# Kernel tuning notes

Hardware: AMD Instinct MI355X
Metric: run time of the kernel (lower is better)

Reference implementation:

```python
import jax, jax.numpy as jnp
import numpy as np

DIM = 1024
HEAD = 16
HEAD_DIM = DIM // HEAD
SCALE = HEAD_DIM ** -0.5
EPS = 1e-5


def layernorm(x, g, b):
    mu = jnp.mean(x, axis=-1, keepdims=True)
    var = jnp.var(x, axis=-1, keepdims=True)
    return (x - mu) * jax.lax.rsqrt(var + EPS) * g + b


def setup_inputs() -> dict:
    key = jax.random.key(0)
    ks = jax.random.split(key, 12)
    B, L = 2, 2048
    s = 0.02
    inp = {
        "x": jax.random.normal(ks[0], (B, L, DIM), jnp.float32),
        "seq_mask": jnp.zeros((B, L), jnp.bool_),
        "wq": jax.random.normal(ks[1], (DIM, DIM), jnp.float32) * s,
        "wk": jax.random.normal(ks[2], (DIM, DIM), jnp.float32) * s,
        "wv": jax.random.normal(ks[3], (DIM, DIM), jnp.float32) * s,
        "wo": jax.random.normal(ks[4], (DIM, DIM), jnp.float32) * s,
        "g1": jnp.ones((DIM,), jnp.float32),
        "b1": jnp.zeros((DIM,), jnp.float32),
        "g2": jnp.ones((DIM,), jnp.float32),
        "b2": jnp.zeros((DIM,), jnp.float32),
        "w_mlp1": jax.random.normal(ks[5], (4 * DIM, DIM), jnp.float32) * s,
        "b_mlp1": jnp.zeros((4 * DIM,), jnp.float32),
        "w_mlp2": jax.random.normal(ks[6], (DIM, 4 * DIM), jnp.float32) * s,
        "b_mlp2": jnp.zeros((DIM,), jnp.float32),
    }
    return inp


def reference(x, seq_mask, wq, wk, wv, wo, g1, b1, g2, b2, w_mlp1, b_mlp1, w_mlp2, b_mlp2):
    B, L, D = x.shape
    # --- pre-norm attention ---
    nx = layernorm(x, g1, b1)
    # torch Linear: y = x @ W.T
    q = (nx @ wq.T).reshape(B, L, HEAD, HEAD_DIM).transpose(0, 2, 1, 3)  # [B,H,L,d]
    k = (nx @ wk.T).reshape(B, L, HEAD, HEAD_DIM).transpose(0, 2, 1, 3)
    v = (nx @ wv.T).reshape(B, L, HEAD, HEAD_DIM).transpose(0, 2, 1, 3)
    scores = jnp.einsum("bhqd,bhkd->bhqk", q, k) * SCALE  # [B,H,L,L]
    causal = jnp.triu(jnp.ones((L, L), jnp.bool_), k=1)  # True = masked
    mask = causal[None, :, :] | seq_mask[:, None, :]      # [B,L,L]
    scores = jnp.where(mask[:, None, :, :], -10000.0, scores)
    attn = jax.nn.softmax(scores, axis=-1)
    out = jnp.einsum("bhqk,bhkd->bhqd", attn, v)
    out = out.transpose(0, 2, 1, 3).reshape(B, L, D)
    attn_out = out @ wo.T
    x = x + attn_out
    # --- pre-norm MLP ---
    nx = layernorm(x, g2, b2)
    h = jax.nn.gelu(nx @ w_mlp1.T + b_mlp1, approximate=False)
    mlp_out = h @ w_mlp2.T + b_mlp2
    return x + mlp_out
```

## Files before the change

### kernel.cpp

```cpp
#include <hip/hip_runtime.h>
#include <hip/hip_bf16.h>
#include <math.h>


#define DIMN 1024
#define NHEAD 16
#define HDIM 64
#define SEQ 2048
#define NTOK 4096
#define QKV_N 3072
#define PADW 72

typedef float v4f __attribute__((ext_vector_type(4)));
typedef short v8s __attribute__((ext_vector_type(8)));

__device__ __forceinline__ float b2f(unsigned short u) {
    union { unsigned int i; float f; } v; v.i = ((unsigned int)u) << 16; return v.f;
}
__device__ __forceinline__ unsigned short f2b(float f) {
    union { float f; unsigned int i; } v; v.f = f;
    unsigned int u = v.i;
    return (unsigned short)((u + 0x7fffu + ((u >> 16) & 1u)) >> 16);
}
__device__ __forceinline__ ushort4 f4tob4(float4 f) {
    ushort4 u; u.x = f2b(f.x); u.y = f2b(f.y); u.z = f2b(f.z); u.w = f2b(f.w); return u;
}
__device__ __forceinline__ void gl2lds16(const unsigned short* g, unsigned short* l) {
    __builtin_amdgcn_global_load_lds(
        (const __attribute__((address_space(1))) unsigned int*)g,
        (__attribute__((address_space(3))) unsigned int*)l, 16, 0, 0);
}

__global__ __launch_bounds__(256) void cast_w_kernel(
    const float* __restrict__ in, unsigned short* __restrict__ out)
{
    size_t i = ((size_t)blockIdx.x * 256 + threadIdx.x) * 8;
    float4 f0 = *(const float4*)(in + i);
    float4 f1 = *(const float4*)(in + i + 4);
    *(ushort4*)(out + i)     = f4tob4(f0);
    *(ushort4*)(out + i + 4) = f4tob4(f1);
}

__global__ __launch_bounds__(256) void concat_w_kernel(
    const float* __restrict__ wq, const float* __restrict__ wk,
    const float* __restrict__ wv, unsigned short* __restrict__ wqkv)
{
    size_t i = ((size_t)blockIdx.x * 256 + threadIdx.x) * 8;
    int which = (int)(i >> 20);
    size_t m = i & ((size_t)(1 << 20) - 1);
    const float* src = (which == 0) ? wq : (which == 1) ? wk : wv;
    float4 f0 = *(const float4*)(src + m);
    float4 f1 = *(const float4*)(src + m + 4);
    *(ushort4*)(wqkv + i)     = f4tob4(f0);
    *(ushort4*)(wqkv + i + 4) = f4tob4(f1);
}

__global__ __launch_bounds__(256) void ln_kernel(
    const float* __restrict__ xin, const float* __restrict__ g,
    const float* __restrict__ b, unsigned short* __restrict__ y)
{
    const int row = blockIdx.x;
    const int t = threadIdx.x;
    float4 u = *((const float4*)(xin + (size_t)row * DIMN) + t);
    float v[4] = {u.x, u.y, u.z, u.w};
    float s1 = v[0] + v[1] + v[2] + v[3];
    float s2 = v[0]*v[0] + v[1]*v[1] + v[2]*v[2] + v[3]*v[3];
    #pragma unroll
    for (int m = 32; m >= 1; m >>= 1) { s1 += __shfl_xor(s1, m); s2 += __shfl_xor(s2, m); }
    __shared__ float a1[4], a2[4];
    const int wave = t >> 6;
    if ((t & 63) == 0) { a1[wave] = s1; a2[wave] = s2; }
    __syncthreads();
    const float S1 = a1[0] + a1[1] + a1[2] + a1[3];
    const float S2 = a2[0] + a2[1] + a2[2] + a2[3];
    const float mean = S1 * (1.0f / DIMN);
    const float var  = S2 * (1.0f / DIMN) - mean * mean;
    const float rinv = rsqrtf(fmaxf(var, 0.0f) + 1e-5f);
    float4 gv = *((const float4*)g + t);
    float4 bv = *((const float4*)b + t);
    ushort4 o;
    o.x = f2b((v[0] - mean) * rinv * gv.x + bv.x);
    o.y = f2b((v[1] - mean) * rinv * gv.y + bv.y);
    o.z = f2b((v[2] - mean) * rinv * gv.z + bv.z);
    o.w = f2b((v[3] - mean) * rinv * gv.w + bv.w);
    *(ushort4*)(y + (size_t)row * DIMN + t * 4) = o;
}

__global__ __launch_bounds__(256) void vtrans_kernel(
    const unsigned short* __restrict__ qkv, unsigned short* __restrict__ vt)
{
    __shared__ unsigned short T[64 * PADW];
    const int st = blockIdx.x;
    const int bh = blockIdx.y;
    const int bb = bh >> 4, h = bh & 15;
    const int t = threadIdx.x;
    const int sr = t >> 2, sc = (t & 3) * 16;
    {
        const unsigned short* g = qkv + (size_t)(bb * SEQ + st * 64 + sr) * QKV_N
                                  + 2 * DIMN + h * HDIM + sc;
        *(uint4*)&T[sr * PADW + sc]     = *(const uint4*)g;
        *(uint4*)&T[sr * PADW + sc + 8] = *(const uint4*)(g + 8);
    }
    __syncthreads();
    {
        const int dr = t >> 2, ss = (t & 3) * 16;
        union { uint4 u; unsigned short s[8]; } o0, o1;
        #pragma unroll
        for (int j = 0; j < 8; j++) o0.s[j] = T[(ss + j) * PADW + dr];
        #pragma unroll
        for (int j = 0; j < 8; j++) o1.s[j] = T[(ss + 8 + j) * PADW + dr];
        unsigned short* dst = vt + ((size_t)bh * 64 + dr) * SEQ + st * 64 + ss;
        *(uint4*)dst       = o0.u;
        *(uint4*)(dst + 8) = o1.u;
    }
}

template<int BN, bool BIAS, bool GELU_ACT, bool RESF32, int OUT>
__global__ __launch_bounds__(256) void gemm_bt_kernel(
    const unsigned short* __restrict__ A, const unsigned short* __restrict__ W,
    const float* __restrict__ bias, const float* __restrict__ resid,
    void* __restrict__ Cout, int M, int N, int K, int LDW)
{
    constexpr int PSA = 128 * 32;
    constexpr int PSB = BN * 32;
    constexpr int TM  = (BN == 128) ? 4 : 2;
    __shared__ unsigned short As[2 * PSA];
    __shared__ unsigned short Bs[2 * PSB];
    const int t = threadIdx.x;
    const int bm = blockIdx.x, bn = blockIdx.y;
    const int wave = t >> 6, lane = t & 63;
    const int lrow = lane & 15, quad = lane >> 4;
    const int wm = (BN == 128) ? (wave & 1) * 64 : wave * 32;
    const int wn = (BN == 128) ? (wave >> 1) * 64 : 0;

    const unsigned short* Ag = A + (size_t)(bm * 128 + (t >> 2)) * K   + (t & 3) * 8;
    const unsigned short* Wg = W + (size_t)(bn * BN  + (t >> 2)) * LDW + (t & 3) * 8;

    v4f acc[TM][4];
    const v4f vzero = {0.f, 0.f, 0.f, 0.f};
    #pragma unroll
    for (int i = 0; i < TM; i++)
        #pragma unroll
        for (int j = 0; j < 4; j++) acc[i][j] = vzero;

    for (int kt = 0; kt < K; kt += 64) {
        gl2lds16(Ag + kt,                        &As[t * 8]);
        gl2lds16(Ag + (size_t)64 * K + kt,       &As[2048 + t * 8]);
        gl2lds16(Ag + kt + 32,                   &As[PSA + t * 8]);
        gl2lds16(Ag + (size_t)64 * K + kt + 32,  &As[PSA + 2048 + t * 8]);
        if constexpr (BN == 128) {
            gl2lds16(Wg + kt,                         &Bs[t * 8]);
            gl2lds16(Wg + (size_t)64 * LDW + kt,      &Bs[2048 + t * 8]);
            gl2lds16(Wg + kt + 32,                    &Bs[PSB + t * 8]);
            gl2lds16(Wg + (size_t)64 * LDW + kt + 32, &Bs[PSB + 2048 + t * 8]);
        } else {
            gl2lds16(Wg + kt,      &Bs[t * 8]);
            gl2lds16(Wg + kt + 32, &Bs[PSB + t * 8]);
        }
        __syncthreads();
        #pragma unroll
        for (int p = 0; p < 2; p++) {
            v8s a[TM], b[4];
            #pragma unroll
            for (int tm = 0; tm < TM; tm++)
                a[tm] = *(const v8s*)&As[p * PSA + (wm + tm * 16 + lrow) * 32 + quad * 8];
            #pragma unroll
            for (int tn = 0; tn < 4; tn++)
                b[tn] = *(const v8s*)&Bs[p * PSB + (wn + tn * 16 + lrow) * 32 + quad * 8];
            #pragma unroll
            for (int tm = 0; tm < TM; tm++)
                #pragma unroll
                for (int tn = 0; tn < 4; tn++)
                    acc[tm][tn] = __builtin_amdgcn_mfma_f32_16x16x32_bf16(
                        a[tm], b[tn], acc[tm][tn], 0, 0, 0);
        }
        __syncthreads();
    }

    #pragma unroll
    for (int tm = 0; tm < TM; tm++) {
        #pragma unroll
        for (int r = 0; r < 4; r++) {
            const int row = bm * 128 + wm + tm * 16 + quad * 4 + r;
            #pragma unroll
            for (int tn = 0; tn < 4; tn++) {
                const int col = bn * BN + wn + tn * 16 + lrow;
                float v = acc[tm][tn][r];
                if (BIAS) v += bias[col];
                if (GELU_ACT) v = 0.5f * v * (1.0f + erff(v * 0.70710678118654752f));
                if (RESF32) v += resid[(size_t)row * N + col];
                if (OUT == 0) ((unsigned short*)Cout)[(size_t)row * N + col] = f2b(v);
                else          ((float*)Cout)[(size_t)row * N + col] = v;
            }
        }
    }
}

__global__ __launch_bounds__(256, 4) void attn_kernel(
    const unsigned short* __restrict__ qkv, const unsigned short* __restrict__ vt,
    unsigned short* __restrict__ aout)
{
    __shared__ unsigned short Qs [64 * PADW];
    __shared__ unsigned short Ks [64 * PADW];
    __shared__ unsigned short Vts[64 * PADW];
    __shared__ unsigned short Ps [64 * PADW];

    const int bh = blockIdx.x;
    const int qt = 31 - blockIdx.y;
    const int bb = bh >> 4, h = bh & 15;
    const int q0 = qt * 64;
    const int t = threadIdx.x;
    const int wave = t >> 6, lane = t & 63;
    const int lrow = lane & 15, quad = lane >> 4;
    const int wq0 = wave * 16;
    const int rotl = (lrow >> 2) & 3;

    const int sr = t >> 2;
    const int sc = (t & 3) * 16;

    {
        const unsigned short* g = qkv + (size_t)(bb * SEQ + q0 + sr) * QKV_N + h * HDIM + sc;
        *(uint4*)&Qs[sr * PADW + sc]     = *(const uint4*)g;
        *(uint4*)&Qs[sr * PADW + sc + 8] = *(const uint4*)(g + 8);
    }

    const unsigned short* kbase = qkv + (size_t)(bb * SEQ + sr) * QKV_N + DIMN + h * HDIM + sc;
    const unsigned short* vbase = vt + ((size_t)bh * 64 + sr) * SEQ + sc;
    uint4 kf0 = *(const uint4*)kbase;
    uint4 kf1 = *(const uint4*)(kbase + 8);
    uint4 vf0 = *(const uint4*)vbase;
    uint4 vf1 = *(const uint4*)(vbase + 8);

    const v4f vzero = {0.f, 0.f, 0.f, 0.f};
    v4f oacc[4], oaccl;
    #pragma unroll
    for (int d = 0; d < 4; d++) oacc[d] = vzero;
    oaccl = vzero;
    v8s bones;
    #pragma unroll
    for (int j = 0; j < 8; j++) bones[j] = (short)0x3F80;

    for (int kti = 0; kti <= qt; kti++) {
        const int kt = kti * 64;
        __syncthreads();
        *(uint4*)&Ks[sr * PADW + sc]      = kf0;
        *(uint4*)&Ks[sr * PADW + sc + 8]  = kf1;
        *(uint4*)&Vts[sr * PADW + sc]     = vf0;
        *(uint4*)&Vts[sr * PADW + sc + 8] = vf1;
        __syncthreads();
        if (kti < qt) {
            const unsigned short* kn = kbase + (size_t)(kti + 1) * 64 * QKV_N;
            const unsigned short* vn = vbase + (kti + 1) * 64;
            kf0 = *(const uint4*)kn;
            kf1 = *(const uint4*)(kn + 8);
            vf0 = *(const uint4*)vn;
            vf1 = *(const uint4*)(vn + 8);
        }

        v8s kb[2][4];
        #pragma unroll
        for (int ks2 = 0; ks2 < 2; ks2++)
            #pragma unroll
            for (int n = 0; n < 4; n++)
                kb[ks2][n] = *(const v8s*)&Ks[(n * 16 + lrow) * PADW + ks2 * 32 + quad * 8];
        v4f sacc[4];
        #pragma unroll
        for (int n = 0; n < 4; n++) sacc[n] = vzero;
        #pragma unroll
        for (int ks2 = 0; ks2 < 2; ks2++) {
            v8s a = *(const v8s*)&Qs[(wq0 + lrow) * PADW + ks2 * 32 + quad * 8];
            #pragma unroll
            for (int n = 0; n < 4; n++)
                sacc[n] = __builtin_amdgcn_mfma_f32_16x16x32_bf16(
                    a, kb[ks2][n], sacc[n], 0, 0, 0);
        }

        const bool diag = (kti == qt);
        #pragma unroll
        for (int n = 0; n < 4; n++) {
            #pragma unroll
            for (int r = 0; r < 4; r++) {
                float e = __expf(fminf(sacc[n][r] * 0.125f, 24.0f));
                if (diag && (n * 16 + lrow) > (wq0 + quad * 4 + r)) e = 0.0f;
                Ps[(wq0 + quad * 4 + r) * PADW + ((n + quad) & 3) * 16 + lrow] = f2b(e);
            }
        }

        v8s vb[2][4];
        #pragma unroll
        for (int ks2 = 0; ks2 < 2; ks2++)
            #pragma unroll
            for (int d = 0; d < 4; d++)
                vb[ks2][d] = *(const v8s*)&Vts[(d * 16 + lrow) * PADW + ks2 * 32 + quad * 8];
        #pragma unroll
        for (int ks2 = 0; ks2 < 2; ks2++) {
            const int kb16 = ks2 * 2 + (quad >> 1);
            v8s a = *(const v8s*)&Ps[(wq0 + lrow) * PADW
                                     + ((kb16 + rotl) & 3) * 16 + (quad & 1) * 8];
            #pragma unroll
            for (int d = 0; d < 4; d++)
                oacc[d] = __builtin_amdgcn_mfma_f32_16x16x32_bf16(
                    a, vb[ks2][d], oacc[d], 0, 0, 0);
            oaccl = __builtin_amdgcn_mfma_f32_16x16x32_bf16(a, bones, oaccl, 0, 0, 0);
        }
    }

    __syncthreads();
    #pragma unroll
    for (int r = 0; r < 4; r++) {
        const float rinv = 1.0f / oaccl[r];
        #pragma unroll
        for (int d = 0; d < 4; d++)
            Qs[(wq0 + quad * 4 + r) * PADW + d * 16 + lrow] = f2b(oacc[d][r] * rinv);
    }
    __syncthreads();
    {
        unsigned short* dst = aout + (size_t)(bb * SEQ + q0 + sr) * DIMN + h * HDIM + sc;
        *(uint4*)dst       = *(const uint4*)&Qs[sr * PADW + sc];
        *(uint4*)(dst + 8) = *(const uint4*)&Qs[sr * PADW + sc + 8];
    }
}

extern "C" void kernel_launch(void* const* d_in, const int* in_sizes, int n_in,
                              void* d_out, int out_size, void* d_ws, size_t ws_size,
                              hipStream_t stream)
{
    const float* x   = (const float*)d_in[0];
    const float* wq  = (const float*)d_in[2];
    const float* wk  = (const float*)d_in[3];
    const float* wv  = (const float*)d_in[4];
    const float* wo  = (const float*)d_in[5];
    const float* g1  = (const float*)d_in[6];
    const float* b1  = (const float*)d_in[7];
    const float* g2  = (const float*)d_in[8];
    const float* b2  = (const float*)d_in[9];
    const float* w1  = (const float*)d_in[10];
    const float* bm1 = (const float*)d_in[11];
    const float* w2  = (const float*)d_in[12];
    const float* bm2 = (const float*)d_in[13];
    float* out = (float*)d_out;

    char* ws = (char*)d_ws;
    const size_t MB = (size_t)1 << 20;
    unsigned short* nx   = (unsigned short*)(ws + 0);
    unsigned short* vtg  = (unsigned short*)(ws + 0);
    unsigned short* nx2  = (unsigned short*)(ws + 0);
    unsigned short* wqkv = (unsigned short*)(ws + 8  * MB);
    unsigned short* wob  = (unsigned short*)(ws + 8  * MB);
    unsigned short* w1b  = (unsigned short*)(ws + 10 * MB);
    unsigned short* w2b  = (unsigned short*)(ws + 18 * MB);
    unsigned short* qkv  = (unsigned short*)(ws + 14 * MB);
    unsigned short* hbuf = (unsigned short*)(ws + 26 * MB);
    unsigned short* aout = (unsigned short*)(ws + 38 * MB);
    float*          x1   = (float*)        (ws + 46 * MB);

    concat_w_kernel<<<1536, 256, 0, stream>>>(wq, wk, wv, wqkv);
    ln_kernel<<<NTOK, 256, 0, stream>>>(x, g1, b1, nx);
    gemm_bt_kernel<128, false, false, false, 0><<<dim3(32, 24), 256, 0, stream>>>(
        nx, wqkv, nullptr, nullptr, qkv, NTOK, QKV_N, DIMN, DIMN);
    vtrans_kernel<<<dim3(32, 32), 256, 0, stream>>>(qkv, vtg);
    cast_w_kernel<<<512, 256, 0, stream>>>(wo, wob);
    attn_kernel<<<dim3(32, 32), 256, 0, stream>>>(qkv, vtg, aout);
    cast_w_kernel<<<2048, 256, 0, stream>>>(w1, w1b);
    cast_w_kernel<<<2048, 256, 0, stream>>>(w2, w2b);
    gemm_bt_kernel<64, false, false, true, 1><<<dim3(32, 16), 256, 0, stream>>>(
        aout, wob, nullptr, x, x1, NTOK, DIMN, DIMN, DIMN);
    ln_kernel<<<NTOK, 256, 0, stream>>>(x1, g2, b2, nx2);
    gemm_bt_kernel<128, true, true, false, 0><<<dim3(32, 16), 256, 0, stream>>>(
        nx2, w1b, bm1, nullptr, hbuf, NTOK, 2048, DIMN, DIMN);
    gemm_bt_kernel<64, false, false, true, 1><<<dim3(32, 16), 256, 0, stream>>>(
        hbuf, w2b, nullptr, x1, out, NTOK, DIMN, 2048, 4 * DIMN);
    gemm_bt_kernel<128, true, true, false, 0><<<dim3(32, 16), 256, 0, stream>>>(
        nx2, w1b + (size_t)2048 * DIMN, bm1 + 2048, nullptr, hbuf, NTOK, 2048, DIMN, DIMN);
    gemm_bt_kernel<64, true, false, true, 1><<<dim3(32, 16), 256, 0, stream>>>(
        hbuf, w2b + 2048, bm2, out, out, NTOK, DIMN, 2048, 4 * DIMN);
}
```

Measured before the change: 371.7 us.

## Merge weight casts, fold softmax scale into Q, store x1 as bf16, widen MLP1

```diff
diff --git a/kernel.cpp b/kernel.cpp
--- a/kernel.cpp
+++ b/kernel.cpp
@@ -22,6 +22,10 @@
     unsigned int u = v.i;
     return (unsigned short)((u + 0x7fffu + ((u >> 16) & 1u)) >> 16);
 }
+__device__ __forceinline__ unsigned short f2b_fast(float f) {
+    union { float f; unsigned int i; } v; v.f = f;
+    return (unsigned short)((v.i + 0x8000u) >> 16);
+}
 __device__ __forceinline__ ushort4 f4tob4(float4 f) {
     ushort4 u; u.x = f2b(f.x); u.y = f2b(f.y); u.z = f2b(f.z); u.w = f2b(f.w); return u;
 }
@@ -30,39 +34,70 @@
         (const __attribute__((address_space(1))) unsigned int*)g,
         (__attribute__((address_space(3))) unsigned int*)l, 16, 0, 0);
 }
-
-__global__ __launch_bounds__(256) void cast_w_kernel(
-    const float* __restrict__ in, unsigned short* __restrict__ out)
-{
-    size_t i = ((size_t)blockIdx.x * 256 + threadIdx.x) * 8;
-    float4 f0 = *(const float4*)(in + i);
-    float4 f1 = *(const float4*)(in + i + 4);
-    *(ushort4*)(out + i)     = f4tob4(f0);
-    *(ushort4*)(out + i + 4) = f4tob4(f1);
-}
-
-__global__ __launch_bounds__(256) void concat_w_kernel(
+__device__ __forceinline__ uint4 scaleq8(uint4 u) {
+    union { uint4 v; unsigned short s[8]; } a; a.v = u;
+    #pragma unroll
+    for (int j = 0; j < 8; j++) a.s[j] = f2b(b2f(a.s[j]) * 0.125f);
+    return a.v;
+}
+
+__global__ __launch_bounds__(256) void prep_w_kernel(
     const float* __restrict__ wq, const float* __restrict__ wk,
-    const float* __restrict__ wv, unsigned short* __restrict__ wqkv)
-{
-    size_t i = ((size_t)blockIdx.x * 256 + threadIdx.x) * 8;
-    int which = (int)(i >> 20);
-    size_t m = i & ((size_t)(1 << 20) - 1);
-    const float* src = (which == 0) ? wq : (which == 1) ? wk : wv;
-    float4 f0 = *(const float4*)(src + m);
-    float4 f1 = *(const float4*)(src + m + 4);
-    *(ushort4*)(wqkv + i)     = f4tob4(f0);
-    *(ushort4*)(wqkv + i + 4) = f4tob4(f1);
-}
-
+    const float* __restrict__ wv, const float* __restrict__ w1,
+    const float* __restrict__ w2, const float* __restrict__ wo,
+    unsigned short* __restrict__ wqkv, unsigned short* __restrict__ w1b,
+    unsigned short* __restrict__ w2b_a, unsigned short* __restrict__ wob)
+{
+    size_t gid = (size_t)blockIdx.x * 256 + threadIdx.x;
+    const float* src; unsigned short* dst; size_t si, di;
+    if (gid < 393216) {
+        size_t i = gid * 8;
+        int which = (int)(i >> 20);
+        src = (which == 0) ? wq : (which == 1) ? wk : wv;
+        si = i & ((size_t)(1 << 20) - 1); dst = wqkv; di = i;
+    } else if (gid < 393216 + 524288) {
+        size_t i = (gid - 393216) * 8;
+        src = w1; si = i; dst = w1b; di = i;
+    } else if (gid < 393216 + 524288 + 262144) {
+        size_t j = (gid - 393216 - 524288) * 8;
+        size_t r = j >> 11, c = j & 2047;
+        src = w2; si = r * 4096 + c; dst = w2b_a; di = j;
+    } else {
+        size_t i = (gid - 393216 - 524288 - 262144) * 8;
+        src = wo; si = i; dst = wob; di = i;
+    }
+    float4 f0 = *(const float4*)(src + si);
+    float4 f1 = *(const float4*)(src + si + 4);
+    *(ushort4*)(dst + di)     = f4tob4(f0);
+    *(ushort4*)(dst + di + 4) = f4tob4(f1);
+}
+
+__global__ __launch_bounds__(256) void cast_w2b_kernel(
+    const float* __restrict__ w2, unsigned short* __restrict__ w2b_b)
+{
+    size_t j = ((size_t)blockIdx.x * 256 + threadIdx.x) * 8;
+    size_t r = j >> 11, c = j & 2047;
+    float4 f0 = *(const float4*)(w2 + r * 4096 + 2048 + c);
+    float4 f1 = *(const float4*)(w2 + r * 4096 + 2048 + c + 4);
+    *(ushort4*)(w2b_b + j)     = f4tob4(f0);
+    *(ushort4*)(w2b_b + j + 4) = f4tob4(f1);
+}
+
+template<int IN>
 __global__ __launch_bounds__(256) void ln_kernel(
-    const float* __restrict__ xin, const float* __restrict__ g,
+    const void* __restrict__ xin, const float* __restrict__ g,
     const float* __restrict__ b, unsigned short* __restrict__ y)
 {
     const int row = blockIdx.x;
     const int t = threadIdx.x;
-    float4 u = *((const float4*)(xin + (size_t)row * DIMN) + t);
-    float v[4] = {u.x, u.y, u.z, u.w};
+    float v[4];
+    if (IN == 1) {
+        float4 u = *((const float4*)((const float*)xin + (size_t)row * DIMN) + t);
+        v[0] = u.x; v[1] = u.y; v[2] = u.z; v[3] = u.w;
+    } else {
+        ushort4 u = *((const ushort4*)((const unsigned short*)xin + (size_t)row * DIMN) + t);
+        v[0] = b2f(u.x); v[1] = b2f(u.y); v[2] = b2f(u.z); v[3] = b2f(u.w);
+    }
     float s1 = v[0] + v[1] + v[2] + v[3];
     float s2 = v[0]*v[0] + v[1]*v[1] + v[2]*v[2] + v[3]*v[3];
     #pragma unroll
@@ -115,11 +150,11 @@
     }
 }
 
-template<int BN, bool BIAS, bool GELU_ACT, bool RESF32, int OUT>
+template<int BN, bool BIAS, bool GELU_ACT, int RES, int OUT>
 __global__ __launch_bounds__(256) void gemm_bt_kernel(
     const unsigned short* __restrict__ A, const unsigned short* __restrict__ W,
-    const float* __restrict__ bias, const float* __restrict__ resid,
-    void* __restrict__ Cout, int M, int N, int K, int LDW)
+    const float* __restrict__ bias, const void* __restrict__ resid,
+    void* __restrict__ Cout, int M, int N, int K, int LDA, int LDW)
 {
     constexpr int PSA = 128 * 32;
     constexpr int PSB = BN * 32;
@@ -133,7 +168,7 @@
     const int wm = (BN == 128) ? (wave & 1) * 64 : wave * 32;
     const int wn = (BN == 128) ? (wave >> 1) * 64 : 0;
 
-    const unsigned short* Ag = A + (size_t)(bm * 128 + (t >> 2)) * K   + (t & 3) * 8;
+    const unsigned short* Ag = A + (size_t)(bm * 128 + (t >> 2)) * LDA + (t & 3) * 8;
     const unsigned short* Wg = W + (size_t)(bn * BN  + (t >> 2)) * LDW + (t & 3) * 8;
 
     v4f acc[TM][4];
@@ -144,10 +179,10 @@
         for (int j = 0; j < 4; j++) acc[i][j] = vzero;
 
     for (int kt = 0; kt < K; kt += 64) {
-        gl2lds16(Ag + kt,                        &As[t * 8]);
-        gl2lds16(Ag + (size_t)64 * K + kt,       &As[2048 + t * 8]);
-        gl2lds16(Ag + kt + 32,                   &As[PSA + t * 8]);
-        gl2lds16(Ag + (size_t)64 * K + kt + 32,  &As[PSA + 2048 + t * 8]);
+        gl2lds16(Ag + kt,                         &As[t * 8]);
+        gl2lds16(Ag + (size_t)64 * LDA + kt,      &As[2048 + t * 8]);
+        gl2lds16(Ag + kt + 32,                    &As[PSA + t * 8]);
+        gl2lds16(Ag + (size_t)64 * LDA + kt + 32, &As[PSA + 2048 + t * 8]);
         if constexpr (BN == 128) {
             gl2lds16(Wg + kt,                         &Bs[t * 8]);
             gl2lds16(Wg + (size_t)64 * LDW + kt,      &Bs[2048 + t * 8]);
@@ -188,7 +223,8 @@
                 float v = acc[tm][tn][r];
                 if (BIAS) v += bias[col];
                 if (GELU_ACT) v = 0.5f * v * (1.0f + erff(v * 0.70710678118654752f));
-                if (RESF32) v += resid[(size_t)row * N + col];
+                if (RES == 1) v += ((const float*)resid)[(size_t)row * N + col];
+                if (RES == 2) v += b2f(((const unsigned short*)resid)[(size_t)row * N + col]);
                 if (OUT == 0) ((unsigned short*)Cout)[(size_t)row * N + col] = f2b(v);
                 else          ((float*)Cout)[(size_t)row * N + col] = v;
             }
@@ -220,8 +256,8 @@
 
     {
         const unsigned short* g = qkv + (size_t)(bb * SEQ + q0 + sr) * QKV_N + h * HDIM + sc;
-        *(uint4*)&Qs[sr * PADW + sc]     = *(const uint4*)g;
-        *(uint4*)&Qs[sr * PADW + sc + 8] = *(const uint4*)(g + 8);
+        *(uint4*)&Qs[sr * PADW + sc]     = scaleq8(*(const uint4*)g);
+        *(uint4*)&Qs[sr * PADW + sc + 8] = scaleq8(*(const uint4*)(g + 8));
     }
 
     const unsigned short* kbase = qkv + (size_t)(bb * SEQ + sr) * QKV_N + DIMN + h * HDIM + sc;
@@ -280,9 +316,9 @@
         for (int n = 0; n < 4; n++) {
             #pragma unroll
             for (int r = 0; r < 4; r++) {
-                float e = __expf(fminf(sacc[n][r] * 0.125f, 24.0f));
+                float e = __expf(fminf(sacc[n][r], 24.0f));
                 if (diag && (n * 16 + lrow) > (wq0 + quad * 4 + r)) e = 0.0f;
-                Ps[(wq0 + quad * 4 + r) * PADW + ((n + quad) & 3) * 16 + lrow] = f2b(e);
+                Ps[(wq0 + quad * 4 + r) * PADW + ((n + quad) & 3) * 16 + lrow] = f2b_fast(e);
             }
         }
 
@@ -342,36 +378,34 @@
 
     char* ws = (char*)d_ws;
     const size_t MB = (size_t)1 << 20;
-    unsigned short* nx   = (unsigned short*)(ws + 0);
-    unsigned short* vtg  = (unsigned short*)(ws + 0);
-    unsigned short* nx2  = (unsigned short*)(ws + 0);
-    unsigned short* wqkv = (unsigned short*)(ws + 8  * MB);
-    unsigned short* wob  = (unsigned short*)(ws + 8  * MB);
-    unsigned short* w1b  = (unsigned short*)(ws + 10 * MB);
-    unsigned short* w2b  = (unsigned short*)(ws + 18 * MB);
-    unsigned short* qkv  = (unsigned short*)(ws + 14 * MB);
-    unsigned short* hbuf = (unsigned short*)(ws + 26 * MB);
-    unsigned short* aout = (unsigned short*)(ws + 38 * MB);
-    float*          x1   = (float*)        (ws + 46 * MB);
-
-    concat_w_kernel<<<1536, 256, 0, stream>>>(wq, wk, wv, wqkv);
-    ln_kernel<<<NTOK, 256, 0, stream>>>(x, g1, b1, nx);
-    gemm_bt_kernel<128, false, false, false, 0><<<dim3(32, 24), 256, 0, stream>>>(
-        nx, wqkv, nullptr, nullptr, qkv, NTOK, QKV_N, DIMN, DIMN);
+    unsigned short* nx    = (unsigned short*)(ws + 0);
+    unsigned short* vtg   = (unsigned short*)(ws + 0);
+    unsigned short* nx2   = (unsigned short*)(ws + 0);
+    unsigned short* w1b   = (unsigned short*)(ws + 8  * MB);
+    unsigned short* w2b_b = (unsigned short*)(ws + 8  * MB);
+    unsigned short* w2b_a = (unsigned short*)(ws + 16 * MB);
+    unsigned short* wob   = (unsigned short*)(ws + 20 * MB);
+    unsigned short* wqkv  = (unsigned short*)(ws + 22 * MB);
+    unsigned short* x1    = (unsigned short*)(ws + 22 * MB);
+    unsigned short* qkv   = (unsigned short*)(ws + 28 * MB);
+    unsigned short* hbuf  = (unsigned short*)(ws + 30 * MB);
+    unsigned short* aout  = (unsigned short*)(ws + 52 * MB);
+
+    prep_w_kernel<<<5120, 256, 0, stream>>>(wq, wk, wv, w1, w2, wo,
+                                            wqkv, w1b, w2b_a, wob);
+    ln_kernel<1><<<NTOK, 256, 0, stream>>>(x, g1, b1, nx);
+    gemm_bt_kernel<128, false, false, 0, 0><<<dim3(32, 24), 256, 0, stream>>>(
+        nx, wqkv, nullptr, nullptr, qkv, NTOK, QKV_N, DIMN, DIMN, DIMN);
     vtrans_kernel<<<dim3(32, 32), 256, 0, stream>>>(qkv, vtg);
-    cast_w_kernel<<<512, 256, 0, stream>>>(wo, wob);
     attn_kernel<<<dim3(32, 32), 256, 0, stream>>>(qkv, vtg, aout);
-    cast_w_kernel<<<2048, 256, 0, stream>>>(w1, w1b);
-    cast_w_kernel<<<2048, 256, 0, stream>>>(w2, w2b);
-    gemm_bt_kernel<64, false, false, true, 1><<<dim3(32, 16), 256, 0, stream>>>(
-        aout, wob, nullptr, x, x1, NTOK, DIMN, DIMN, DIMN);
-    ln_kernel<<<NTOK, 256, 0, stream>>>(x1, g2, b2, nx2);
-    gemm_bt_kernel<128, true, true, false, 0><<<dim3(32, 16), 256, 0, stream>>>(
-        nx2, w1b, bm1, nullptr, hbuf, NTOK, 2048, DIMN, DIMN);
-    gemm_bt_kernel<64, false, false, true, 1><<<dim3(32, 16), 256, 0, stream>>>(
-        hbuf, w2b, nullptr, x1, out, NTOK, DIMN, 2048, 4 * DIMN);
-    gemm_bt_kernel<128, true, true, false, 0><<<dim3(32, 16), 256, 0, stream>>>(
-        nx2, w1b + (size_t)2048 * DIMN, bm1 + 2048, nullptr, hbuf, NTOK, 2048, DIMN, DIMN);
-    gemm_bt_kernel<64, true, false, true, 1><<<dim3(32, 16), 256, 0, stream>>>(
-        hbuf, w2b + 2048, bm2, out, out, NTOK, DIMN, 2048, 4 * DIMN);
-}
+    gemm_bt_kernel<64, false, false, 1, 0><<<dim3(32, 16), 256, 0, stream>>>(
+        aout, wob, nullptr, x, x1, NTOK, DIMN, DIMN, DIMN, DIMN);
+    ln_kernel<0><<<NTOK, 256, 0, stream>>>(x1, g2, b2, nx2);
+    gemm_bt_kernel<128, true, true, 0, 0><<<dim3(32, 32), 256, 0, stream>>>(
+        nx2, w1b, bm1, nullptr, hbuf, NTOK, 4 * DIMN, DIMN, DIMN, DIMN);
+    cast_w2b_kernel<<<1024, 256, 0, stream>>>(w2, w2b_b);
+    gemm_bt_kernel<64, false, false, 2, 1><<<dim3(32, 16), 256, 0, stream>>>(
+        hbuf, w2b_a, nullptr, x1, out, NTOK, DIMN, 2048, 4 * DIMN, 2048);
+    gemm_bt_kernel<64, true, false, 1, 1><<<dim3(32, 16), 256, 0, stream>>>(
+        hbuf + 2048, w2b_b, bm2, out, out, NTOK, DIMN, 2048, 4 * DIMN, 2048);
+}
```

After: 360.6 us. 3.0% less time.
